# Optimization experiments

Measured on AMD Instinct MI355X. Metric: run time of the kernel, lower is better.

The kernel has to match this reference:

```python
import jax, jax.numpy as jnp
import numpy as np

DMODEL = 1024
N_EXPERTS = 8
EXPERT_SIZE = 4096
TOPK = 2
B, S = 2, 2048


def setup_inputs() -> dict:
    key = jax.random.key(0)
    ks = jax.random.split(key, 6)
    std = EXPERT_SIZE ** (-0.5)  # init_expert_weights: normal(0, expert_size**-0.5 * weight_scale)
    x = jax.random.normal(ks[0], (B, S, DMODEL), dtype=jnp.float32)
    gate_w = 0.02 * jax.random.normal(ks[1], (N_EXPERTS, DMODEL), dtype=jnp.float32)
    w1 = std * jax.random.normal(ks[2], (N_EXPERTS, EXPERT_SIZE, DMODEL), dtype=jnp.float32)
    b1 = jnp.zeros((N_EXPERTS, EXPERT_SIZE), dtype=jnp.float32)
    w2 = std * jax.random.normal(ks[3], (N_EXPERTS, DMODEL, EXPERT_SIZE), dtype=jnp.float32)
    b2 = jnp.zeros((N_EXPERTS, DMODEL), dtype=jnp.float32)
    return {"x": x, "gate_w": gate_w, "w1": w1, "b1": b1, "w2": w2, "b2": b2}


def reference(x, gate_w, w1, b1, w2, b2):
    # Router: gate linear (no bias) -> softmax -> top-k expert selection
    logits = jnp.einsum('bsd,ed->bse', x, gate_w)          # [B,S,E]
    probs = jax.nn.softmax(logits, axis=-1)                # gate_softmax
    top_w, top_i = jax.lax.top_k(probs, TOPK)              # [B,S,K]
    # Scatter top-k weights back to a dense [B,S,E] routing matrix
    route = jnp.sum(jax.nn.one_hot(top_i, N_EXPERTS, dtype=probs.dtype)
                    * top_w[..., None], axis=-2)           # [B,S,E]
    # Per-expert 2-layer MLP (Linear -> ReLU -> Linear), combined by route weights
    out = jnp.zeros_like(x)
    for e in range(N_EXPERTS):
        h = jax.nn.relu(jnp.einsum('bsd,hd->bsh', x, w1[e]) + b1[e])  # [B,S,H]
        y = jnp.einsum('bsh,dh->bsd', h, w2[e]) + b2[e]               # [B,S,D]
        out = out + route[..., e, None] * y
    return out
```

## Files before the change

kernel.cpp:

```cpp
#include <hip/hip_runtime.h>
#include <hip/hip_bf16.h>
#include <stdint.h>

#define DMODEL 1024
#define NEXP   8
#define HSZ    4096
#define NTOK   4096

typedef __attribute__((ext_vector_type(8))) short bf16x8;
typedef __attribute__((ext_vector_type(4))) float f32x4;

__device__ __forceinline__ unsigned short f2bf(float f) {
  union { float f; unsigned u; } v; v.f = f;
  return (unsigned short)((v.u + 0x8000u) >> 16);
}

__device__ __forceinline__ void gl2lds16(const void* g, void* lds) {
  __builtin_amdgcn_global_load_lds(
      (const __attribute__((address_space(1))) unsigned*)g,
      (__attribute__((address_space(3))) unsigned*)lds, 16, 0, 0);
}

__global__ __launch_bounds__(256) void cvt_all_kernel(
    const float* __restrict__ x, const float* __restrict__ w1,
    const float* __restrict__ w2, unsigned short* __restrict__ xb,
    unsigned short* __restrict__ w1b, unsigned short* __restrict__ w2b) {
  const size_t n0 = (size_t)NTOK * DMODEL / 4;
  const size_t n1 = (size_t)NEXP * HSZ * DMODEL / 4;
  size_t i = (size_t)blockIdx.x * 256 + threadIdx.x;
  const float* src; unsigned short* dst; size_t j;
  if (i < n0)            { src = x;  dst = xb;  j = i; }
  else if (i < n0 + n1)  { src = w1; dst = w1b; j = i - n0; }
  else                   { src = w2; dst = w2b; j = i - n0 - n1; }
  float4 v = ((const float4*)src)[j];
  ((ushort4*)dst)[j] = make_ushort4(f2bf(v.x), f2bf(v.y), f2bf(v.z), f2bf(v.w));
}

__global__ __launch_bounds__(256) void router_kernel(
    const float* __restrict__ x, const float* __restrict__ gw,
    int* __restrict__ cnt, int* __restrict__ tokl, float* __restrict__ twgt,
    int* __restrict__ sidx) {
  int wave = threadIdx.x >> 6;
  int lane = threadIdx.x & 63;
  int t = blockIdx.x * 4 + wave;
  const float* xr = x + (size_t)t * DMODEL;
  float acc[NEXP];
#pragma unroll
  for (int e = 0; e < NEXP; ++e) acc[e] = 0.f;
  for (int d = lane; d < DMODEL; d += 64) {
    float xv = xr[d];
#pragma unroll
    for (int e = 0; e < NEXP; ++e) acc[e] = fmaf(xv, gw[e * DMODEL + d], acc[e]);
  }
#pragma unroll
  for (int e = 0; e < NEXP; ++e) {
#pragma unroll
    for (int o = 32; o > 0; o >>= 1) acc[e] += __shfl_down(acc[e], o);
  }
  if (lane == 0) {
    float m = acc[0];
#pragma unroll
    for (int e = 1; e < NEXP; ++e) m = fmaxf(m, acc[e]);
    float p[NEXP]; float s = 0.f;
#pragma unroll
    for (int e = 0; e < NEXP; ++e) { p[e] = __expf(acc[e] - m); s += p[e]; }
    float inv = 1.f / s;
    int i0 = 0; float b0 = p[0];
#pragma unroll
    for (int e = 1; e < NEXP; ++e) if (p[e] > b0) { b0 = p[e]; i0 = e; }
    int i1 = (i0 == 0) ? 1 : 0; float b1v = p[i1];
#pragma unroll
    for (int e = 0; e < NEXP; ++e) if (e != i0 && p[e] > b1v) { b1v = p[e]; i1 = e; }
    int p0 = atomicAdd(&cnt[i0], 1);
    tokl[i0 * NTOK + p0] = t; twgt[i0 * NTOK + p0] = b0 * inv;
    int p1 = atomicAdd(&cnt[i1], 1);
    tokl[i1 * NTOK + p1] = t; twgt[i1 * NTOK + p1] = b1v * inv;
    sidx[2 * t]     = (i0 << 16) | p0;
    sidx[2 * t + 1] = (i1 << 16) | p1;
  }
}

__global__ __launch_bounds__(256) void gemm1_bf_kernel(
    const unsigned short* __restrict__ Xbf, const unsigned short* __restrict__ W1bf,
    const float* __restrict__ b1, const int* __restrict__ cnt,
    const int* __restrict__ tokl, unsigned short* __restrict__ Hbuf) {
  const int e = blockIdx.z;
  const int ne = cnt[e];
  const int m0 = blockIdx.y * 128;
  if (m0 >= ne) return;
  const int n0 = blockIdx.x * 128;
  int toff = 0;
  for (int i = 0; i < NEXP; ++i) toff += (i < e) ? cnt[i] : 0;

  __shared__ __align__(16) unsigned short As[128 * 32];
  __shared__ __align__(16) unsigned short Bs[128 * 32];

  const int tid = threadIdx.x;
  const int lane = tid & 63;
  const int wave = tid >> 6;
  const int wm = (wave >> 1) * 64;
  const int wn = (wave & 1) * 64;

  const int srow = wave * 16 + (lane >> 2);
  const int scol = (lane & 3) * 8;
  const int* tlist = tokl + e * NTOK;
  const unsigned short* gA[2]; const unsigned short* gB[2];
  unsigned short* lA[2]; unsigned short* lB[2];
#pragma unroll
  for (int c = 0; c < 2; ++c) {
    int r = c * 64 + srow;
    int gr = m0 + r;
    int tk = tlist[(gr < ne) ? gr : 0];
    gA[c] = Xbf + (size_t)tk * DMODEL + scol;
    gB[c] = W1bf + (size_t)e * HSZ * DMODEL + (size_t)(n0 + r) * DMODEL + scol;
    lA[c] = &As[(c * 64 + wave * 16) * 32];
    lB[c] = &Bs[(c * 64 + wave * 16) * 32];
  }

  f32x4 acc[4][4];
#pragma unroll
  for (int i = 0; i < 4; ++i)
#pragma unroll
    for (int j = 0; j < 4; ++j) acc[i][j] = (f32x4){0.f, 0.f, 0.f, 0.f};

  const int fr = lane & 15;
  const int fk = (lane >> 4) * 8;

  for (int k0 = 0; k0 < DMODEL; k0 += 32) {
    __syncthreads();
#pragma unroll
    for (int c = 0; c < 2; ++c) {
      gl2lds16(gA[c] + k0, lA[c]);
      gl2lds16(gB[c] + k0, lB[c]);
    }
    __syncthreads();
    bf16x8 af[4], bfg[4];
#pragma unroll
    for (int i = 0; i < 4; ++i) {
      af[i]  = *(const bf16x8*)&As[(wm + i * 16 + fr) * 32 + fk];
      bfg[i] = *(const bf16x8*)&Bs[(wn + i * 16 + fr) * 32 + fk];
    }
#pragma unroll
    for (int i = 0; i < 4; ++i)
#pragma unroll
      for (int j = 0; j < 4; ++j)
        acc[i][j] = __builtin_amdgcn_mfma_f32_16x16x32_bf16(bfg[j], af[i], acc[i][j], 0, 0, 0);
  }

  const int hq = (lane >> 4) * 4;
#pragma unroll
  for (int i = 0; i < 4; ++i) {
    int trow = m0 + wm + i * 16 + fr;
    if (trow >= ne) continue;
    size_t hrow = (size_t)(toff + trow) * HSZ;
#pragma unroll
    for (int j = 0; j < 4; ++j) {
      int hcol = n0 + wn + j * 16 + hq;
      const float* bp = b1 + e * HSZ + hcol;
      unsigned short u[4];
#pragma unroll
      for (int r = 0; r < 4; ++r)
        u[r] = f2bf(fmaxf(acc[i][j][r] + bp[r], 0.f));
      *(ushort4*)&Hbuf[hrow + hcol] = make_ushort4(u[0], u[1], u[2], u[3]);
    }
  }
}

__global__ __launch_bounds__(256) void gemm2_bf_kernel(
    const unsigned short* __restrict__ Hbuf, const unsigned short* __restrict__ W2bf,
    const float* __restrict__ b2, const int* __restrict__ cnt,
    const float* __restrict__ twgt, float* __restrict__ Ybuf) {
  const int e = blockIdx.z;
  const int ne = cnt[e];
  const int m0 = blockIdx.y * 128;
  if (m0 >= ne) return;
  const int n0 = blockIdx.x * 128;
  int toff = 0;
  for (int i = 0; i < NEXP; ++i) toff += (i < e) ? cnt[i] : 0;

  __shared__ __align__(16) unsigned short As[128 * 64];
  __shared__ __align__(16) unsigned short Bs[128 * 64];

  const int tid = threadIdx.x;
  const int lane = tid & 63;
  const int wave = tid >> 6;
  const int wm = (wave >> 1) * 64;
  const int wn = (wave & 1) * 64;

  const int srow = (wave << 5) + (lane >> 3);
  const int scb  = (((lane & 7) ^ (lane >> 3)) << 3);
  const unsigned short* gA[4]; const unsigned short* gB[4];
  unsigned short* lA[4]; unsigned short* lB[4];
#pragma unroll
  for (int c = 0; c < 4; ++c) {
    int r = srow + c * 8;
    int gr = m0 + r;
    int rc = (gr < ne) ? gr : 0;
    gA[c] = Hbuf + (size_t)(toff + rc) * HSZ + scb;
    gB[c] = W2bf + (size_t)e * DMODEL * HSZ + (size_t)(n0 + r) * HSZ + scb;
    lA[c] = &As[((wave << 5) + c * 8) * 64];
    lB[c] = &Bs[((wave << 5) + c * 8) * 64];
  }

  f32x4 acc[4][4];
#pragma unroll
  for (int i = 0; i < 4; ++i)
#pragma unroll
    for (int j = 0; j < 4; ++j) acc[i][j] = (f32x4){0.f, 0.f, 0.f, 0.f};

  const int fr = lane & 15;
  const int cb0 = lane >> 4;

  for (int k0 = 0; k0 < HSZ; k0 += 64) {
    __syncthreads();
#pragma unroll
    for (int c = 0; c < 4; ++c) {
      gl2lds16(gA[c] + k0, lA[c]);
      gl2lds16(gB[c] + k0, lB[c]);
    }
    __syncthreads();
    bf16x8 af[2][4], bfg[2][4];
#pragma unroll
    for (int h = 0; h < 2; ++h) {
      int cb = cb0 + h * 4;
#pragma unroll
      for (int i = 0; i < 4; ++i) {
        int ar = wm + i * 16 + fr;
        af[h][i]  = *(const bf16x8*)&As[ar * 64 + ((cb ^ (ar & 7)) << 3)];
        int br = wn + i * 16 + fr;
        bfg[h][i] = *(const bf16x8*)&Bs[br * 64 + ((cb ^ (br & 7)) << 3)];
      }
    }
#pragma unroll
    for (int h = 0; h < 2; ++h)
#pragma unroll
      for (int i = 0; i < 4; ++i)
#pragma unroll
        for (int j = 0; j < 4; ++j)
          acc[i][j] = __builtin_amdgcn_mfma_f32_16x16x32_bf16(bfg[h][j], af[h][i],
                                                              acc[i][j], 0, 0, 0);
  }

  const float* wlist = twgt + e * NTOK;
  const int dq = (lane >> 4) * 4;
#pragma unroll
  for (int i = 0; i < 4; ++i) {
    int trow = m0 + wm + i * 16 + fr;
    if (trow >= ne) continue;
    float wgt = wlist[trow];
    float* yrow = Ybuf + (size_t)(toff + trow) * DMODEL;
#pragma unroll
    for (int j = 0; j < 4; ++j) {
      int d0 = n0 + wn + j * 16 + dq;
      const float* b2p = b2 + e * DMODEL + d0;
      float4 v = make_float4(wgt * (acc[i][j][0] + b2p[0]),
                             wgt * (acc[i][j][1] + b2p[1]),
                             wgt * (acc[i][j][2] + b2p[2]),
                             wgt * (acc[i][j][3] + b2p[3]));
      *(float4*)(yrow + d0) = v;
    }
  }
}

__global__ __launch_bounds__(256) void combine_kernel(
    const float* __restrict__ Ybuf, const int* __restrict__ cnt,
    const int* __restrict__ sidx, float* __restrict__ out) {
  int t = blockIdx.x;
  int offv[NEXP];
  int s = 0;
#pragma unroll
  for (int e = 0; e < NEXP; ++e) { offv[e] = s; s += cnt[e]; }
  int s0 = sidx[2 * t], s1 = sidx[2 * t + 1];
  size_t r0 = (size_t)(offv[s0 >> 16] + (s0 & 0xffff)) * DMODEL;
  size_t r1 = (size_t)(offv[s1 >> 16] + (s1 & 0xffff)) * DMODEL;
  int c = threadIdx.x * 4;
  float4 a = *(const float4*)(Ybuf + r0 + c);
  float4 b = *(const float4*)(Ybuf + r1 + c);
  *(float4*)(out + (size_t)t * DMODEL + c) =
      make_float4(a.x + b.x, a.y + b.y, a.z + b.z, a.w + b.w);
}

extern "C" void kernel_launch(void* const* d_in, const int* in_sizes, int n_in,
                              void* d_out, int out_size, void* d_ws, size_t ws_size,
                              hipStream_t stream) {
  const float* x  = (const float*)d_in[0];
  const float* gw = (const float*)d_in[1];
  const float* w1 = (const float*)d_in[2];
  const float* b1 = (const float*)d_in[3];
  const float* w2 = (const float*)d_in[4];
  const float* b2 = (const float*)d_in[5];
  float* out = (float*)d_out;

  char* ws = (char*)d_ws;
  int* cnt    = (int*)ws;
  int* tokl   = (int*)(ws + 128);
  float* twgt = (float*)(ws + 128 + NEXP * NTOK * 4);
  int* sidx   = (int*)(ws + 128 + 2 * NEXP * NTOK * 4);

  constexpr size_t OFF_XBF  = 327680;
  constexpr size_t OFF_W1BF = OFF_XBF  + (size_t)NTOK * DMODEL * 2;
  constexpr size_t OFF_W2BF = OFF_W1BF + (size_t)NEXP * HSZ * DMODEL * 2;
  constexpr size_t OFF_HBUF = OFF_W2BF + (size_t)NEXP * DMODEL * HSZ * 2;
  unsigned short* Xbf  = (unsigned short*)(ws + OFF_XBF);
  unsigned short* W1bf = (unsigned short*)(ws + OFF_W1BF);
  unsigned short* W2bf = (unsigned short*)(ws + OFF_W2BF);
  unsigned short* Hbuf = (unsigned short*)(ws + OFF_HBUF);
  float* Ybuf = (float*)(ws + OFF_W1BF);

  hipMemsetAsync(cnt, 0, 32, stream);
  router_kernel<<<NTOK / 4, 256, 0, stream>>>(x, gw, cnt, tokl, twgt, sidx);
  const size_t ncvt = (size_t)NTOK * DMODEL / 4 + 2 * (size_t)NEXP * HSZ * DMODEL / 4;
  cvt_all_kernel<<<(unsigned)((ncvt + 255) / 256), 256, 0, stream>>>(
      x, w1, w2, Xbf, W1bf, W2bf);
  gemm1_bf_kernel<<<dim3(HSZ / 128, NTOK / 128, NEXP), 256, 0, stream>>>(
      Xbf, W1bf, b1, cnt, tokl, Hbuf);
  gemm2_bf_kernel<<<dim3(DMODEL / 128, NTOK / 128, NEXP), 256, 0, stream>>>(
      Hbuf, W2bf, b2, cnt, twgt, Ybuf);
  combine_kernel<<<NTOK, 256, 0, stream>>>(Ybuf, cnt, sidx, out);
}
```

Measured before the change: 669.1 us.

## Double-buffer LDS tiles in both expert GEMMs and swizzle GEMM1 LDS layout

Both expert GEMM kernels now keep two LDS buffers per operand. The next K-slice is issued with global_load_lds while MFMAs run on the current slice, which drops one barrier per iteration and overlaps global loads with compute. GEMM1 also gets an XOR column swizzle on its 32-wide LDS rows, applied consistently on store and fragment read, to reduce bank conflicts. LDS use per block doubles (64KB for GEMM2), which may cut how many blocks fit per CU.

```diff
diff --git a/kernel.cpp b/kernel.cpp
--- a/kernel.cpp
+++ b/kernel.cpp
@@ -92,8 +92,8 @@
   int toff = 0;
   for (int i = 0; i < NEXP; ++i) toff += (i < e) ? cnt[i] : 0;
 
-  __shared__ __align__(16) unsigned short As[128 * 32];
-  __shared__ __align__(16) unsigned short Bs[128 * 32];
+  __shared__ __align__(16) unsigned short As[2][128 * 32];
+  __shared__ __align__(16) unsigned short Bs[2][128 * 32];
 
   const int tid = threadIdx.x;
   const int lane = tid & 63;
@@ -102,10 +102,10 @@
   const int wn = (wave & 1) * 64;
 
   const int srow = wave * 16 + (lane >> 2);
-  const int scol = (lane & 3) * 8;
+  const int scol = (((lane & 3) ^ ((lane >> 3) & 3)) << 3);
   const int* tlist = tokl + e * NTOK;
   const unsigned short* gA[2]; const unsigned short* gB[2];
-  unsigned short* lA[2]; unsigned short* lB[2];
+  int lofs[2];
 #pragma unroll
   for (int c = 0; c < 2; ++c) {
     int r = c * 64 + srow;
@@ -113,8 +113,7 @@
     int tk = tlist[(gr < ne) ? gr : 0];
     gA[c] = Xbf + (size_t)tk * DMODEL + scol;
     gB[c] = W1bf + (size_t)e * HSZ * DMODEL + (size_t)(n0 + r) * DMODEL + scol;
-    lA[c] = &As[(c * 64 + wave * 16) * 32];
-    lB[c] = &Bs[(c * 64 + wave * 16) * 32];
+    lofs[c] = (c * 64 + wave * 16) * 32;
   }
 
   f32x4 acc[4][4];
@@ -124,27 +123,40 @@
     for (int j = 0; j < 4; ++j) acc[i][j] = (f32x4){0.f, 0.f, 0.f, 0.f};
 
   const int fr = lane & 15;
-  const int fk = (lane >> 4) * 8;
-
+  const int cb = lane >> 4;
+
+#pragma unroll
+  for (int c = 0; c < 2; ++c) {
+    gl2lds16(gA[c], &As[0][lofs[c]]);
+    gl2lds16(gB[c], &Bs[0][lofs[c]]);
+  }
+  __syncthreads();
+
+  int cur = 0;
   for (int k0 = 0; k0 < DMODEL; k0 += 32) {
-    __syncthreads();
-#pragma unroll
-    for (int c = 0; c < 2; ++c) {
-      gl2lds16(gA[c] + k0, lA[c]);
-      gl2lds16(gB[c] + k0, lB[c]);
-    }
-    __syncthreads();
+    const int nxt = k0 + 32;
+    if (nxt < DMODEL) {
+#pragma unroll
+      for (int c = 0; c < 2; ++c) {
+        gl2lds16(gA[c] + nxt, &As[cur ^ 1][lofs[c]]);
+        gl2lds16(gB[c] + nxt, &Bs[cur ^ 1][lofs[c]]);
+      }
+    }
     bf16x8 af[4], bfg[4];
 #pragma unroll
     for (int i = 0; i < 4; ++i) {
-      af[i]  = *(const bf16x8*)&As[(wm + i * 16 + fr) * 32 + fk];
-      bfg[i] = *(const bf16x8*)&Bs[(wn + i * 16 + fr) * 32 + fk];
+      int ar = wm + i * 16 + fr;
+      af[i]  = *(const bf16x8*)&As[cur][ar * 32 + ((cb ^ ((ar >> 1) & 3)) << 3)];
+      int br = wn + i * 16 + fr;
+      bfg[i] = *(const bf16x8*)&Bs[cur][br * 32 + ((cb ^ ((br >> 1) & 3)) << 3)];
     }
 #pragma unroll
     for (int i = 0; i < 4; ++i)
 #pragma unroll
       for (int j = 0; j < 4; ++j)
         acc[i][j] = __builtin_amdgcn_mfma_f32_16x16x32_bf16(bfg[j], af[i], acc[i][j], 0, 0, 0);
+    __syncthreads();
+    cur ^= 1;
   }
 
   const int hq = (lane >> 4) * 4;
@@ -178,8 +190,8 @@
   int toff = 0;
   for (int i = 0; i < NEXP; ++i) toff += (i < e) ? cnt[i] : 0;
 
-  __shared__ __align__(16) unsigned short As[128 * 64];
-  __shared__ __align__(16) unsigned short Bs[128 * 64];
+  __shared__ __align__(16) unsigned short As[2][128 * 64];
+  __shared__ __align__(16) unsigned short Bs[2][128 * 64];
 
   const int tid = threadIdx.x;
   const int lane = tid & 63;
@@ -190,7 +202,7 @@
   const int srow = (wave << 5) + (lane >> 3);
   const int scb  = (((lane & 7) ^ (lane >> 3)) << 3);
   const unsigned short* gA[4]; const unsigned short* gB[4];
-  unsigned short* lA[4]; unsigned short* lB[4];
+  int lofs[4];
 #pragma unroll
   for (int c = 0; c < 4; ++c) {
     int r = srow + c * 8;
@@ -198,8 +210,7 @@
     int rc = (gr < ne) ? gr : 0;
     gA[c] = Hbuf + (size_t)(toff + rc) * HSZ + scb;
     gB[c] = W2bf + (size_t)e * DMODEL * HSZ + (size_t)(n0 + r) * HSZ + scb;
-    lA[c] = &As[((wave << 5) + c * 8) * 64];
-    lB[c] = &Bs[((wave << 5) + c * 8) * 64];
+    lofs[c] = ((wave << 5) + c * 8) * 64;
   }
 
   f32x4 acc[4][4];
@@ -211,14 +222,23 @@
   const int fr = lane & 15;
   const int cb0 = lane >> 4;
 
+#pragma unroll
+  for (int c = 0; c < 4; ++c) {
+    gl2lds16(gA[c], &As[0][lofs[c]]);
+    gl2lds16(gB[c], &Bs[0][lofs[c]]);
+  }
+  __syncthreads();
+
+  int cur = 0;
   for (int k0 = 0; k0 < HSZ; k0 += 64) {
-    __syncthreads();
-#pragma unroll
-    for (int c = 0; c < 4; ++c) {
-      gl2lds16(gA[c] + k0, lA[c]);
-      gl2lds16(gB[c] + k0, lB[c]);
-    }
-    __syncthreads();
+    const int nxt = k0 + 64;
+    if (nxt < HSZ) {
+#pragma unroll
+      for (int c = 0; c < 4; ++c) {
+        gl2lds16(gA[c] + nxt, &As[cur ^ 1][lofs[c]]);
+        gl2lds16(gB[c] + nxt, &Bs[cur ^ 1][lofs[c]]);
+      }
+    }
     bf16x8 af[2][4], bfg[2][4];
 #pragma unroll
     for (int h = 0; h < 2; ++h) {
@@ -226,9 +246,9 @@
 #pragma unroll
       for (int i = 0; i < 4; ++i) {
         int ar = wm + i * 16 + fr;
-        af[h][i]  = *(const bf16x8*)&As[ar * 64 + ((cb ^ (ar & 7)) << 3)];
+        af[h][i]  = *(const bf16x8*)&As[cur][ar * 64 + ((cb ^ (ar & 7)) << 3)];
         int br = wn + i * 16 + fr;
-        bfg[h][i] = *(const bf16x8*)&Bs[br * 64 + ((cb ^ (br & 7)) << 3)];
+        bfg[h][i] = *(const bf16x8*)&Bs[cur][br * 64 + ((cb ^ (br & 7)) << 3)];
       }
     }
 #pragma unroll
@@ -239,6 +259,8 @@
         for (int j = 0; j < 4; ++j)
           acc[i][j] = __builtin_amdgcn_mfma_f32_16x16x32_bf16(bfg[h][j], af[h][i],
                                                               acc[i][j], 0, 0, 0);
+    __syncthreads();
+    cur ^= 1;
   }
 
   const float* wlist = twgt + e * NTOK;
```

Result: no change. 673.8 us (+0.7%).
